# Kernel tuning notes

Hardware: AMD Instinct MI355X
Metric: run time of the kernel (lower is better)

## Reference

```python
import jax, jax.numpy as jnp
import numpy as np

OBS, PRED = 8, 12
EIN, EHID, NOISE = 64, 256, 64
GEMB = 64
DHID = EHID + NOISE  # 320
G, NPER = 8, 192
B = G * NPER


def leaky(x):
    return jnp.where(x > 0, x, 0.2 * x)


def lstm_cell(x, h, c, Wih, Whh, bih, bhh):
    gates = x @ Wih.T + bih + h @ Whh.T + bhh
    i, f, g, o = jnp.split(gates, 4, axis=-1)
    c = jax.nn.sigmoid(f) * c + jax.nn.sigmoid(i) * jnp.tanh(g)
    h = jax.nn.sigmoid(o) * jnp.tanh(c)
    return h, c


def kmeans(x, k, niter=10):
    # deterministic init: first k points (torch used randperm)
    c = x[:k]
    ar = jnp.arange(k)
    for _ in range(niter):
        d2 = ((x[:, None, :] - c[None, :, :]) ** 2).sum(-1)  # [N,k]
        a = jnp.argmin(d2, axis=1)
        onehot = (a[:, None] == ar[None, :]).astype(x.dtype)  # [N,k]
        cnt = onehot.sum(0)
        mean = (onehot.T @ x) / jnp.maximum(cnt, 1.0)[:, None]
        c = jnp.where((cnt == 0)[:, None], x[:k], mean)  # reseed dead clusters
    d2 = ((x[:, None, :] - c[None, :, :]) ** 2).sum(-1)
    return jnp.argmin(d2, axis=1)


def signed_graph(node, W_ne, b_ne, W_att, b_att):
    n, D = node.shape
    emb = node @ W_ne.T + b_ne  # [n,E]
    E = emb.shape[1]
    a_other, a_self = W_att[0, :E], W_att[0, E:]
    # e[i,j] = a_other.emb[j] + a_self.emb[i] + b  (cat([other, self]) order)
    e = (emb @ a_other)[None, :] + (emb @ a_self)[:, None] + b_att[0]
    edge = jax.nn.softmax(leaky(e), axis=0)
    edge = jnp.triu(edge, 0) + jnp.triu(edge, 1).T  # symmetrize from upper tri
    d = edge.sum(1)
    L = jnp.diag(d) - edge
    dinv = 1.0 / jnp.sqrt(d)
    L_sym = dinv[:, None] * L * dinv[None, :]
    lam, H = jnp.linalg.eigh(jax.lax.stop_gradient(L_sym))  # ascending eigvals
    H = H[:, :2]  # two smallest
    Hn = H / jnp.sqrt((H ** 2).sum(1, keepdims=True))
    labels = kmeans(Hn, int(np.ceil(n / 2)))
    same = labels[:, None] == labels[None, :]
    NEG = jnp.float32(-1e8)
    pos_alpha = jax.nn.softmax(leaky(edge * jnp.where(same, 1.0, NEG)), axis=0)
    neg_alpha = jax.nn.softmax(leaky(edge * jnp.where(same, NEG, 1.0)), axis=0)
    feat = jax.nn.relu(pos_alpha[..., None] * node[None, :, :]) + \
           jax.nn.relu(neg_alpha[..., None] * node[None, :, :])  # [n,n,D]
    return feat.sum(axis=1)


def setup_inputs():
    key = jax.random.key(0)
    ks = jax.random.split(key, 22)
    p = lambda k, s: jax.random.normal(k, s, jnp.float32) * 0.1
    starts = jnp.arange(G, dtype=jnp.int32) * NPER
    return {
        "input_traj": jax.random.normal(ks[0], (OBS + PRED, B, 2), jnp.float32),
        "enc_h0": jax.random.normal(ks[1], (B, EHID), jnp.float32),
        "enc_c0": jax.random.normal(ks[2], (B, EHID), jnp.float32),
        "noise_z": jax.random.normal(ks[3], (G, NOISE), jnp.float32),
        "W_emb": p(ks[4], (EIN, 2)), "b_emb": p(ks[5], (EIN,)),
        "Wih_e": p(ks[6], (4 * EHID, EIN)), "Whh_e": p(ks[7], (4 * EHID, EHID)),
        "bih_e": p(ks[8], (4 * EHID,)), "bhh_e": p(ks[9], (4 * EHID,)),
        "Wih_d": p(ks[10], (4 * DHID, EIN)), "Whh_d": p(ks[11], (4 * DHID, DHID)),
        "bih_d": p(ks[12], (4 * DHID,)), "bhh_d": p(ks[13], (4 * DHID,)),
        "W_out": p(ks[14], (2, DHID)), "b_out": p(ks[15], (2,)),
        "W_ne": p(ks[16], (GEMB, DHID)), "b_ne": p(ks[17], (GEMB,)),
        "W_att": p(ks[18], (1, 2 * GEMB)), "b_att": p(ks[19], (1,)),
        "seq_start_end": jnp.stack([starts, starts + NPER], axis=1),
    }


def reference(input_traj, enc_h0, enc_c0, noise_z, W_emb, b_emb,
              Wih_e, Whh_e, bih_e, bhh_e, Wih_d, Whh_d, bih_d, bhh_d,
              W_out, b_out, W_ne, b_ne, W_att, b_att, seq_start_end):
    # ---- encoder ----
    x = jax.nn.relu(input_traj @ W_emb.T + b_emb)  # [T,B,EIN]
    def step(carry, xt):
        h, c = carry
        h, c = lstm_cell(xt, h, c, Wih_e, Whh_e, bih_e, bhh_e)
        return (h, c), None
    (h_enc, _), _ = jax.lax.scan(step, (enc_h0, enc_c0), x[:OBS])
    # ---- add per-scene noise (equal-sized scenes) ----
    z = jnp.repeat(noise_z, NPER, axis=0)  # [B,NOISE]
    h = jnp.concatenate([h_enc, z], axis=1)  # [B,DHID]
    c = jnp.zeros_like(h)
    traj_out = input_traj[OBS - 1]  # [B,2]
    sg = jax.vmap(lambda nd: signed_graph(nd, W_ne, b_ne, W_att, b_att))
    preds = []
    for i in range(PRED):  # eval mode: no teacher forcing
        inp = jax.nn.relu(traj_out @ W_emb.T + b_emb)
        if i % 12 == 4:
            h = sg(h.reshape(G, NPER, DHID)).reshape(B, DHID)
        h, c = lstm_cell(inp, h, c, Wih_d, Whh_d, bih_d, bhh_d)
        traj_out = h @ W_out.T + b_out
        preds.append(traj_out)
    return jnp.stack(preds)  # [PRED,B,2]
```

## Files before the change

### kernel.cpp

```cpp
#include <hip/hip_runtime.h>
#include <hip/hip_bf16.h>

typedef __hip_bfloat16 bf16;

#define NN 192
#define NG 8
#define BB 1536
#define EHID 256
#define DH 320
#define PRED 12
#define STRD 192
#define ATILE (NN*STRD)

__device__ __forceinline__ int aoffc(int r, int c){
  int c4 = c >> 2;
  int s = (c4 & ~7) | ((c4 + 3*r) & 7);
  return r*STRD + (s << 2) + (c & 3);
}

#define WAVE_SYNC() do { asm volatile("" ::: "memory"); __builtin_amdgcn_wave_barrier(); } while (0)

__device__ __forceinline__ float waveSum(float v){
#pragma unroll
  for (int o = 32; o > 0; o >>= 1) v += __shfl_down(v, o);
  return v;
}
__device__ __forceinline__ double waveSumD(double v){
#pragma unroll
  for (int o = 32; o > 0; o >>= 1) v += __shfl_down(v, o);
  return v;
}
__device__ __forceinline__ float waveAllSum(float v){
#pragma unroll
  for (int o = 32; o > 0; o >>= 1) v += __shfl_xor(v, o);
  return v;
}
__device__ __forceinline__ double waveAllSumD(double v){
#pragma unroll
  for (int o = 32; o > 0; o >>= 1) v += __shfl_xor(v, o);
  return v;
}

__device__ __forceinline__ double blockSumD(double v, double* red){
  int lane = threadIdx.x & 63, wid = threadIdx.x >> 6, nw = (int)blockDim.x >> 6;
  double s = waveSumD(v);
  __syncthreads();
  if (lane == 0) red[wid] = s;
  __syncthreads();
  if (wid == 0){
    double t = (lane < nw) ? red[lane] : 0.0;
    t = waveSumD(t);
    if (lane == 0) red[0] = t;
  }
  __syncthreads();
  return red[0];
}


__global__ void k_zero_int(int* __restrict__ p, int n){
  int i = blockIdx.x*blockDim.x + threadIdx.x;
  if (i < n) p[i] = 0;
}
__global__ void k_zero_f(float* __restrict__ p, int n){
  int i = blockIdx.x*blockDim.x + threadIdx.x;
  if (i < n) p[i] = 0.f;
}

__global__ void k_probe(const unsigned short* __restrict__ src, int n, int* __restrict__ cnt){
  int tid = blockIdx.x*blockDim.x + threadIdx.x;
  int stride = gridDim.x*blockDim.x;
  int bad = 0;
  for (int j = tid; j < n; j += stride){
    float v = __uint_as_float(((unsigned int)src[j]) << 16);
    if (!(fabsf(v) < 100.f)) bad++;
  }
#pragma unroll
  for (int o = 32; o > 0; o >>= 1) bad += __shfl_down(bad, o);
  if ((threadIdx.x & 63) == 0 && bad > 0) atomicAdd(cnt, bad);
}
__global__ void k_flag(const int* __restrict__ cnt, int* __restrict__ flag){
  *flag = (*cnt > 4096) ? 1 : 0;
}

struct CvtArgs {
  const void* src[20];
  float*      dst[20];
  int         n[20];
};

__global__ void k_convert(CvtArgs a, const int* __restrict__ flag){
  int id = blockIdx.y;
  int n = a.n[id];
  float* d = a.dst[id];
  int t = blockIdx.x*blockDim.x + threadIdx.x;
  int stride = gridDim.x*blockDim.x;
  if (*flag == 0){
    const bf16* s = (const bf16*)a.src[id];
    for (int j = t; j < n; j += stride) d[j] = __bfloat162float(s[j]);
  } else {
    const float* s = (const float*)a.src[id];
    for (int j = t; j < n; j += stride) d[j] = s[j];
  }
}


__global__ void k_embed(const float* __restrict__ in, const float* __restrict__ W,
                        const float* __restrict__ b, float* __restrict__ out){
  int r = blockIdx.x, e = threadIdx.x;
  float x = in[r*2], y = in[r*2+1];
  float v = W[e*2]*x + W[e*2+1]*y + b[e];
  out[r*64+e] = v > 0.f ? v : 0.f;
}

__global__ void k_concat(const float* __restrict__ henc, const float* __restrict__ z,
                         float* __restrict__ h){
  int idx = blockIdx.x*blockDim.x + threadIdx.x;
  if (idx >= BB*DH) return;
  int b = idx / DH, j = idx - b*DH;
  h[idx] = (j < EHID) ? henc[b*EHID + j] : z[(b/NN)*64 + (j - EHID)];
}

__global__ void k_copy_f(const float* __restrict__ in, float* __restrict__ dst, int n){
  int i = blockIdx.x*blockDim.x + threadIdx.x;
  if (i < n) dst[i] = in[i];
}

__global__ __launch_bounds__(256) void k_gates(
    const float* __restrict__ A1, const float* __restrict__ W1, int K1,
    const float* __restrict__ A2, const float* __restrict__ W2, int K2,
    const float* __restrict__ b1, const float* __restrict__ b2,
    float* __restrict__ C, int N){
  __shared__ __align__(16) float As[32][68];
  __shared__ __align__(16) float Ws[32][68];
  int tid = threadIdx.x;
  int tx = tid & 15, ty = tid >> 4;
  int n0 = blockIdx.x * 64, m0 = blockIdx.y * 64;
  float acc[4][4] = {};
  for (int ph = 0; ph < 2; ++ph){
    const float* A = ph ? A2 : A1;
    const float* W = ph ? W2 : W1;
    int K = ph ? K2 : K1;
    for (int k0 = 0; k0 < K; k0 += 32){
      {
        int am = tid >> 2, ak = (tid & 3) * 8;
        const float* srcA = A + (size_t)(m0+am)*K + k0 + ak;
        float4 f0 = *(const float4*)(srcA);
        float4 f1 = *(const float4*)(srcA+4);
        As[ak+0][am]=f0.x; As[ak+1][am]=f0.y; As[ak+2][am]=f0.z; As[ak+3][am]=f0.w;
        As[ak+4][am]=f1.x; As[ak+5][am]=f1.y; As[ak+6][am]=f1.z; As[ak+7][am]=f1.w;
        const float* srcW = W + (size_t)(n0+am)*K + k0 + ak;
        float4 w0 = *(const float4*)(srcW);
        float4 w1 = *(const float4*)(srcW+4);
        Ws[ak+0][am]=w0.x; Ws[ak+1][am]=w0.y; Ws[ak+2][am]=w0.z; Ws[ak+3][am]=w0.w;
        Ws[ak+4][am]=w1.x; Ws[ak+5][am]=w1.y; Ws[ak+6][am]=w1.z; Ws[ak+7][am]=w1.w;
      }
      __syncthreads();
#pragma unroll
      for (int k = 0; k < 32; ++k){
        float4 a0 = *(const float4*)&As[k][ty*4];
        float4 b0 = *(const float4*)&Ws[k][tx*4];
        float av[4] = {a0.x, a0.y, a0.z, a0.w};
        float bv[4] = {b0.x, b0.y, b0.z, b0.w};
#pragma unroll
        for (int i = 0; i < 4; ++i)
#pragma unroll
          for (int j = 0; j < 4; ++j)
            acc[i][j] += av[i]*bv[j];
      }
      __syncthreads();
    }
  }
  float bs[4];
#pragma unroll
  for (int j = 0; j < 4; ++j){
    int col = n0 + tx*4 + j;
    bs[j] = b1[col] + b2[col];
  }
#pragma unroll
  for (int i = 0; i < 4; ++i){
    int row = m0 + ty*4 + i;
    float4 v;
    v.x = acc[i][0] + bs[0]; v.y = acc[i][1] + bs[1];
    v.z = acc[i][2] + bs[2]; v.w = acc[i][3] + bs[3];
    *(float4*)&C[(size_t)row*N + n0 + tx*4] = v;
  }
}

__global__ void k_lstm(const float* __restrict__ gates, float* __restrict__ c,
                       float* __restrict__ h, int H){
  int idx = blockIdx.x*blockDim.x + threadIdx.x;
  if (idx >= BB*H) return;
  int b = idx / H, j = idx - b*H;
  const float* g = gates + (size_t)b*4*H;
  float gi = g[j], gf = g[H+j], gg = g[2*H+j], go = g[3*H+j];
  float si = 1.f/(1.f+expf(-gi));
  float sf = 1.f/(1.f+expf(-gf));
  float so = 1.f/(1.f+expf(-go));
  float cc = sf*c[idx] + si*tanhf(gg);
  c[idx] = cc;
  h[idx] = so*tanhf(cc);
}

__global__ void k_outproj(const float* __restrict__ h, const float* __restrict__ W,
                          const float* __restrict__ bo, float* __restrict__ traj,
                          void* __restrict__ outbase, int step, const int* __restrict__ flag){
  int b = blockIdx.x, lane = threadIdx.x;
  const float* hb = h + (size_t)b*DH;
  float a0 = 0.f, a1 = 0.f;
  for (int k = lane; k < DH; k += 64){
    float hv = hb[k];
    a0 += hv*W[k];
    a1 += hv*W[DH+k];
  }
  a0 = waveSum(a0); a1 = waveSum(a1);
  if (lane == 0){
    a0 += bo[0]; a1 += bo[1];
    traj[b*2] = a0; traj[b*2+1] = a1;
    size_t idx = (size_t)step*BB*2 + (size_t)b*2;
    if (*flag == 0){
      bf16* o = (bf16*)outbase;
      o[idx] = __float2bfloat16(a0); o[idx+1] = __float2bfloat16(a1);
    } else {
      float* o = (float*)outbase;
      o[idx] = a0; o[idx+1] = a1;
    }
  }
}


__global__ void k_sg_emb(const float* __restrict__ h, const float* __restrict__ Wne,
                         const float* __restrict__ bne, const float* __restrict__ Watt,
                         double* __restrict__ sself, double* __restrict__ sother){
  int node = blockIdx.x, e = threadIdx.x;
  const float* hb = h + (size_t)node*DH;
  double acc = (double)bne[e];
  for (int k = 0; k < DH; ++k) acc += (double)hb[k]*(double)Wne[e*DH+k];
  double po = acc * (double)Watt[e];
  double ps = acc * (double)Watt[64+e];
  po = waveSumD(po); ps = waveSumD(ps);
  if (e == 0){ sother[node] = po; sself[node] = ps; }
}

__global__ void k_sg_edgecol(const double* __restrict__ sself, const double* __restrict__ sother,
                             const float* __restrict__ batt, double* __restrict__ edge){
  int g = blockIdx.x, j = threadIdx.x;
  const double* ss = sself + g*NN;
  double bb = (double)batt[0];
  double sj = sother[g*NN + j];
  double m = -1e300;
  for (int i = 0; i < NN; ++i){
    double e = ss[i] + sj + bb; e = e > 0.0 ? e : 0.2*e;
    m = fmax(m, e);
  }
  double sum = 0.0;
  for (int i = 0; i < NN; ++i){
    double e = ss[i] + sj + bb; e = e > 0.0 ? e : 0.2*e;
    sum += exp(e - m);
  }
  double* E = edge + (size_t)g*NN*NN;
  for (int i = 0; i < NN; ++i){
    double e = ss[i] + sj + bb; e = e > 0.0 ? e : 0.2*e;
    E[i*NN + j] = exp(e - m)/sum;
  }
}

__global__ void k_sg_sym(const double* __restrict__ edge, double* __restrict__ esym){
  int idx = blockIdx.x*blockDim.x + threadIdx.x;
  if (idx >= NG*NN*NN) return;
  int g = idx / (NN*NN), r = idx - g*NN*NN;
  int i = r / NN, j = r - i*NN;
  const double* E = edge + (size_t)g*NN*NN;
  esym[idx] = (i <= j) ? E[i*NN + j] : E[j*NN + i];
}

__global__ void k_sg_dsum(const double* __restrict__ esym, double* __restrict__ darr){
  int i = blockIdx.x*blockDim.x + threadIdx.x;
  if (i >= NG*NN) return;
  int g = i / NN, li = i - g*NN;
  const double* E = esym + (size_t)g*NN*NN + (size_t)li*NN;
  double s = 0.0;
  for (int j = 0; j < NN; ++j) s += E[j];
  darr[i] = fmax(s, 1e-300);
}

__global__ void k_sg_lsym(const double* __restrict__ esym, const double* __restrict__ darr,
                          float* __restrict__ Afull){
  int idx = blockIdx.x*blockDim.x + threadIdx.x;
  if (idx >= NG*NN*NN) return;
  int g = idx / (NN*NN), r = idx - g*NN*NN;
  int i = r / NN, j = r - i*NN;
  double w = esym[idx];
  double lij = (i == j) ? (darr[g*NN+i] - w) : (-w);
  Afull[(size_t)g*ATILE + aoffc(i, j)] =
      (float)(lij / (sqrt(darr[g*NN+i])*sqrt(darr[g*NN+j])));
}

__global__ __launch_bounds__(1024) void k_sg_eigen(const float* __restrict__ Afull,
                                                   const double* __restrict__ darr,
                                                   double* __restrict__ v1out){
  extern __shared__ unsigned char ldsraw[];
  float*  A     = (float*)ldsraw;
  double* dd    = (double*)(ldsraw + 147456);
  double* ee    = dd + NN;
  double* yv    = ee + NN;
  double* lu_d  = yv + NN;
  double* lu_du = lu_d + NN;
  double* lu_du2= lu_du + NN;
  double* redA  = lu_du2 + NN;
  double* redB  = redA + 16;
  double* salpha= redB + 16;
  float*  uu    = (float*)(ldsraw + 156944);
  float*  ww    = uu + NN;
  int*    lu_piv= (int*)(ww + NN);
  float*  pp4   = (float*)yv;
  double* lu_dl = (double*)uu;

  int g = blockIdx.x, tid = threadIdx.x;
  int lane = tid & 63, wid = tid >> 6;
  int rtid = tid & 255, team = tid >> 8;

  const float* src = Afull + (size_t)g*ATILE;
  for (int t = tid*4; t < ATILE; t += 4096) *(float4*)&A[t] = *(const float4*)&src[t];
  __syncthreads();

  for (int k = 0; k < NN-65; ++k){
    int m = NN-1-k;
    int i = k+1+rtid;
    float x = 0.f;
    if (rtid < m) x = A[aoffc(i, k)];
    if (tid == 0) *salpha = (double)x;
    if (team == 0){
      float part = (rtid > 0 && rtid < m) ? x*x : 0.f;
      part = waveSum(part);
      if (lane == 0) redA[wid] = (double)part;
    }
    __syncthreads();
    double sigma = redA[0] + redA[1] + redA[2] + redA[3];
    double alpha = *salpha;
    double beta, tau, scale;
    if (sigma <= 1e-30){ tau = 0.0; beta = alpha; scale = 0.0; }
    else {
      beta = -copysign(sqrt(alpha*alpha + sigma), alpha);
      tau = (beta - alpha)/beta;
      scale = 1.0/(alpha - beta);
    }
    float tau_f = (float)tau, scale_f = (float)scale;
    if (tid == 0){
      dd[k] = (double)A[aoffc(k, k)];
      ee[k] = beta;
      A[aoffc(k, k)] = tau_f;
    }
    if (tau != 0.0){
      float u_i = 0.f;
      if (rtid < m) u_i = (rtid == 0) ? 1.f : x*scale_f;
      if (team == 0 && rtid < m){
        uu[i] = u_i;
        if (rtid >= 1) A[aoffc(i, k)] = u_i;
      }
      __syncthreads();
      int c0 = k+1;
      int cA = (c0+3)&~3;
      int cB = (c0+31)&~31;
      int NB = (NN - cB) >> 5;
      const int rb = i*STRD;
      const int rk3 = (3*i) & 7;
      int off[8];
#pragma unroll
      for (int j = 0; j < 8; ++j) off[j] = ((j + rk3) & 7) << 2;
      if (rtid < m){
        float s0=0.f, s1=0.f, s2=0.f, s3=0.f, accs=0.f;
        if (team == 3){
          int c = c0;
          for (; c < cA; ++c) accs += A[aoffc(i, c)]*uu[c];
          for (; c < cB; c += 4){
            int c4 = c>>2; int s = (c4&~7)|((c4+rk3)&7);
            float4 a4 = *(const float4*)&A[rb + (s<<2)];
            float4 u4 = *(const float4*)&uu[c];
            s0 += a4.x*u4.x; s1 += a4.y*u4.y; s2 += a4.z*u4.z; s3 += a4.w*u4.w;
          }
        }
        for (int b = team; b < NB; b += 4){
          int c = cB + (b<<5);
          const int cb = rb + c;
#pragma unroll
          for (int j = 0; j < 8; ++j){
            float4 a4 = *(const float4*)&A[cb + off[j]];
            float4 u4 = *(const float4*)&uu[c + 4*j];
            s0 += a4.x*u4.x; s1 += a4.y*u4.y; s2 += a4.z*u4.z; s3 += a4.w*u4.w;
          }
        }
        pp4[team*NN + i - (k+1) + (k+1)] = ((s0+s1)+(s2+s3)) + accs;
      }
      __syncthreads();
      float p = 0.f;
      if (rtid < m)
        p = tau_f*(pp4[i] + pp4[NN + i] + pp4[2*NN + i] + pp4[3*NN + i]);
      if (team == 0){
        float vp = (rtid < m) ? u_i*p : 0.f;
        vp = waveSum(vp);
        if (lane == 0) redB[wid] = (double)vp;
      }
      __syncthreads();
      double vtp = redB[0] + redB[1] + redB[2] + redB[3];
      float Kc_f = (float)(0.5*tau*vtp);
      float w_i = 0.f;
      if (rtid < m){
        w_i = p - Kc_f*u_i;
        if (team == 0) ww[i] = w_i;
      }
      __syncthreads();
      if (rtid < m){
        if (team == 3){
          int c = c0;
          for (; c < cA; ++c) A[aoffc(i, c)] -= u_i*ww[c] + w_i*uu[c];
          for (; c < cB; c += 4){
            int c4 = c>>2; int s = (c4&~7)|((c4+rk3)&7);
            float* ap = &A[rb + (s<<2)];
            float4 a4 = *(const float4*)ap;
            float4 u4 = *(const float4*)&uu[c];
            float4 w4 = *(const float4*)&ww[c];
            a4.x -= u_i*w4.x + w_i*u4.x;
            a4.y -= u_i*w4.y + w_i*u4.y;
            a4.z -= u_i*w4.z + w_i*u4.z;
            a4.w -= u_i*w4.w + w_i*u4.w;
            *(float4*)ap = a4;
          }
        }
        for (int b = team; b < NB; b += 4){
          int c = cB + (b<<5);
          const int cb = rb + c;
#pragma unroll
          for (int j = 0; j < 8; ++j){
            float* ap = &A[cb + off[j]];
            float4 a4 = *(const float4*)ap;
            float4 u4 = *(const float4*)&uu[c + 4*j];
            float4 w4 = *(const float4*)&ww[c + 4*j];
            a4.x -= u_i*w4.x + w_i*u4.x;
            a4.y -= u_i*w4.y + w_i*u4.y;
            a4.z -= u_i*w4.z + w_i*u4.z;
            a4.w -= u_i*w4.w + w_i*u4.w;
            *(float4*)ap = a4;
          }
        }
      }
      __syncthreads();
    } else {
      __syncthreads();
    }
  }

  if (wid != 0) return;

  for (int k = NN-65; k < NN-2; ++k){
    int m = NN-1-k;
    int i = k+1+lane;
    bool act = lane < m;
    float x = act ? A[aoffc(i, k)] : 0.f;
    float part = (lane > 0) ? x*x : 0.f;
    float sig_f = waveAllSum(part);
    float alpha_f = __shfl(x, 0);
    double sigma = (double)sig_f;
    double alpha = (double)alpha_f;
    double beta, tau, scale;
    if (sigma <= 1e-30){ tau = 0.0; beta = alpha; scale = 0.0; }
    else {
      beta = -copysign(sqrt(alpha*alpha + sigma), alpha);
      tau = (beta - alpha)/beta;
      scale = 1.0/(alpha - beta);
    }
    float tau_f = (float)tau, scale_f = (float)scale;
    if (lane == 0){
      dd[k] = (double)A[aoffc(k, k)];
      ee[k] = beta;
      A[aoffc(k, k)] = tau_f;
    }
    if (tau == 0.0) continue;
    float u = (lane == 0) ? 1.f : x*scale_f;
    int base4 = (k+1) & ~3;
    int ph = (k+1) - base4;
    uu[lane + ph] = u;
    if (lane >= 1 && act) A[aoffc(i, k)] = u;
    WAVE_SYNC();
    int ic = act ? i : (k+1);
    const int rb = ic*STRD;
    const int rk3 = (3*ic) & 7;
    float s0=0.f, s1=0.f, s2=0.f, s3=0.f, accs=0.f;
    {
      int c = k+1;
      int cA = (c+3)&~3; if (cA > NN) cA = NN;
      for (; c < cA; ++c) accs += A[aoffc(ic, c)]*uu[c-base4];
      for (; c < NN; c += 4){
        int c4 = c>>2; int s = (c4&~7)|((c4+rk3)&7);
        float4 a4 = *(const float4*)&A[rb + (s<<2)];
        float4 u4 = *(const float4*)&uu[c-base4];
        s0 += a4.x*u4.x; s1 += a4.y*u4.y; s2 += a4.z*u4.z; s3 += a4.w*u4.w;
      }
    }
    float p = tau_f*(((s0+s1)+(s2+s3)) + accs);
    float vtp = waveAllSum(u*p);
    float Kc_f = (float)(0.5*tau*(double)vtp);
    float w = p - Kc_f*u;
    ww[lane + ph] = w;
    WAVE_SYNC();
    if (act){
      int c = k+1;
      int cA = (c+3)&~3; if (cA > NN) cA = NN;
      for (; c < cA; ++c) A[aoffc(i, c)] -= u*ww[c-base4] + w*uu[c-base4];
      for (; c < NN; c += 4){
        int c4 = c>>2; int s = (c4&~7)|((c4+rk3)&7);
        float* ap = &A[rb + (s<<2)];
        float4 a4 = *(const float4*)ap;
        float4 u4 = *(const float4*)&uu[c-base4];
        float4 w4 = *(const float4*)&ww[c-base4];
        a4.x -= u*w4.x + w*u4.x;
        a4.y -= u*w4.y + w*u4.y;
        a4.z -= u*w4.z + w*u4.z;
        a4.w -= u*w4.w + w*u4.w;
        *(float4*)ap = a4;
      }
    }
    WAVE_SYNC();
  }

  if (lane == 0){
    dd[NN-2] = (double)A[aoffc(NN-2, NN-2)];
    ee[NN-2] = (double)A[aoffc(NN-1, NN-2)];
    dd[NN-1] = (double)A[aoffc(NN-1, NN-1)];
  }
  WAVE_SYNC();

  {
    double mn = 1e300, mx = -1e300;
    for (int i = lane; i < NN; i += 64){
      double r = (i > 0 ? fabs(ee[i-1]) : 0.0) + (i < NN-1 ? fabs(ee[i]) : 0.0);
      mn = fmin(mn, dd[i]-r); mx = fmax(mx, dd[i]+r);
    }
#pragma unroll
    for (int o = 32; o > 0; o >>= 1){
      mn = fmin(mn, __shfl_down(mn, o));
      mx = fmax(mx, __shfl_down(mx, o));
    }
    mn = __shfl(mn, 0); mx = __shfl(mx, 0);
    double lo = mn - 1e-8 - 1e-9*fabs(mn);
    double hi = mx + 1e-8 + 1e-9*fabs(mx);
    for (int it = 0; it < 10; ++it){
      double lam = lo + (hi-lo)*((double)(lane+1)/65.0);
      int cnt = 0;
      double q = dd[0] - lam;
      if (q < 0.0) cnt++;
      for (int i2 = 1; i2 < NN; ++i2){
        double den = q;
        if (fabs(den) < 1e-280) den = (den < 0.0) ? -1e-280 : 1e-280;
        q = dd[i2] - lam - ee[i2-1]*ee[i2-1]/den;
        if (q < 0.0) cnt++;
      }
      unsigned long long bal = __ballot(cnt >= 2);
      if (bal == 0ull){
        lo = lo + (hi-lo)*(64.0/65.0);
      } else {
        int j0 = __ffsll(bal) - 1;
        double nl = lo + (hi-lo)*((double)j0/65.0);
        double nh = lo + (hi-lo)*((double)(j0+1)/65.0);
        lo = nl; hi = nh;
      }
    }
    double lam1 = 0.5*(lo+hi);

    if (lane == 0){
      for (int i = 0; i < NN; ++i) lu_d[i] = dd[i] - lam1;
      for (int i = 0; i < NN-1; ++i){ lu_dl[i] = ee[i]; lu_du[i] = ee[i]; }
      for (int i = 0; i < NN-2; ++i) lu_du2[i] = 0.0;
      for (int i = 0; i < NN-1; ++i){
        if (fabs(lu_d[i]) >= fabs(lu_dl[i])){
          double di = lu_d[i];
          if (fabs(di) < 1e-30){ di = (di < 0.0) ? -1e-30 : 1e-30; lu_d[i] = di; }
          double fact = lu_dl[i]/di;
          lu_dl[i] = fact;
          lu_d[i+1] -= fact*lu_du[i];
          lu_piv[i] = 0;
        } else {
          double fact = lu_d[i]/lu_dl[i];
          lu_d[i] = lu_dl[i];
          double tmp = lu_d[i+1];
          lu_d[i+1] = lu_du[i] - fact*tmp;
          if (i < NN-2){ lu_du2[i] = lu_du[i+1]; lu_du[i+1] = -fact*lu_du[i+1]; }
          lu_du[i] = tmp;
          lu_dl[i] = fact;
          lu_piv[i] = 1;
        }
      }
      if (fabs(lu_d[NN-1]) < 1e-30)
        lu_d[NN-1] = (lu_d[NN-1] < 0.0) ? -1e-30 : 1e-30;
      for (int i = 0; i < NN; ++i) yv[i] = 1.0 + 0.001*(double)((i*37)%29);
      for (int round = 0; round < 2; ++round){
        for (int i = 0; i < NN-1; ++i){
          if (lu_piv[i] == 0){
            yv[i+1] -= lu_dl[i]*yv[i];
          } else {
            double t = yv[i]; yv[i] = yv[i+1]; yv[i+1] = t - lu_dl[i]*yv[i];
          }
        }
        double mx1 = 0.0;
        for (int i = 0; i < NN; ++i) mx1 = fmax(mx1, fabs(yv[i]));
        double inv1 = (mx1 > 0.0 && isfinite(mx1)) ? 1.0/mx1 : 1.0;
        for (int i = 0; i < NN; ++i) yv[i] *= inv1;
        yv[NN-1] = yv[NN-1]/lu_d[NN-1];
        yv[NN-2] = (yv[NN-2] - lu_du[NN-2]*yv[NN-1])/lu_d[NN-2];
        for (int i = NN-3; i >= 0; --i)
          yv[i] = (yv[i] - lu_du[i]*yv[i+1] - lu_du2[i]*yv[i+2])/lu_d[i];
        double mxv = 0.0;
        for (int i = 0; i < NN; ++i) mxv = fmax(mxv, fabs(yv[i]));
        double inv = (mxv > 0.0 && isfinite(mxv)) ? 1.0/mxv : 1.0;
        for (int i = 0; i < NN; ++i){
          double val = yv[i]*inv;
          if (!isfinite(val)) val = 0.0;
          yv[i] = val;
        }
      }
    }
  }
  WAVE_SYNC();

  {
    int r0 = lane, r1 = lane+64, r2 = lane+128;
    double y0 = yv[r0], y1 = yv[r1], y2 = yv[r2];
    for (int k = NN-3; k >= 0; --k){
      double tau = (double)A[aoffc(k, k)];
      if (tau != 0.0){
        double u0 = (r0 > k) ? ((r0 == k+1) ? 1.0 : (double)A[aoffc(r0, k)]) : 0.0;
        double u1 = (r1 > k) ? ((r1 == k+1) ? 1.0 : (double)A[aoffc(r1, k)]) : 0.0;
        double u2 = (r2 > k) ? ((r2 == k+1) ? 1.0 : (double)A[aoffc(r2, k)]) : 0.0;
        double part = u0*y0 + u1*y1 + u2*y2;
        part = waveAllSumD(part);
        double s = tau*part;
        y0 -= s*u0; y1 -= s*u1; y2 -= s*u2;
      }
    }

    const double* dg = darr + (size_t)g*NN;
    double d0 = dg[r0], d1 = dg[r1], d2 = dg[r2];
    double sd0 = sqrt(d0), sd1 = sqrt(d1), sd2 = sqrt(d2);
    double pd  = waveAllSumD(sd0*y0 + sd1*y1 + sd2*y2);
    double pn2 = waveAllSumD(d0 + d1 + d2);
    double coef = pd/fmax(pn2, 1e-300);
    y0 -= coef*sd0; y1 -= coef*sd1; y2 -= coef*sd2;
    double s2 = waveAllSumD(y0*y0 + y1*y1 + y2*y2);
    double nrm = sqrt(s2);
    double inv = (nrm > 0.0 && isfinite(nrm)) ? 1.0/nrm : 0.0;
    double o0 = y0*inv, o1 = y1*inv, o2 = y2*inv;
    if (!isfinite(o0)) o0 = 0.0;
    if (!isfinite(o1)) o1 = 0.0;
    if (!isfinite(o2)) o2 = 0.0;
    v1out[g*NN + r0] = o0;
    v1out[g*NN + r1] = o1;
    v1out[g*NN + r2] = o2;
  }
}

__global__ __launch_bounds__(256) void k_sg_kmeans(const double* __restrict__ darr,
                                                   const double* __restrict__ v1,
                                                   int* __restrict__ labels){
  __shared__ double px[NN], py[NN], cx[96], cy[96];
  __shared__ int lab[NN];
  __shared__ double red[16];
  int g = blockIdx.x, tid = threadIdx.x;
  double part = 0.0;
  for (int i = tid; i < NN; i += 256) part += darr[g*NN + i];
  double sumd = blockSumD(part, red);
  double invn = 1.0/sqrt(fmax(sumd, 1e-300));
  for (int i = tid; i < NN; i += 256){
    double h0 = sqrt(darr[g*NN + i])*invn;
    double h1 = v1[g*NN + i];
    double rn = sqrt(h0*h0 + h1*h1);
    double ax = h0/rn, ay = h1/rn;
    if (!isfinite(ax)) ax = 0.0;
    if (!isfinite(ay)) ay = 0.0;
    px[i] = ax; py[i] = ay;
  }
  __syncthreads();
  if (tid < 96){ cx[tid] = px[tid]; cy[tid] = py[tid]; }
  __syncthreads();
  for (int it = 0; it <= 10; ++it){
    if (tid < NN){
      double bx = px[tid], by = py[tid];
      double best = 1e300; int bi = 0;
      for (int a = 0; a < 96; ++a){
        double dx = bx - cx[a], dy = by - cy[a];
        double d2 = dx*dx + dy*dy;
        if (d2 < best){ best = d2; bi = a; }
      }
      lab[tid] = bi;
    }
    __syncthreads();
    if (it == 10) break;
    if (tid < 96){
      int c = 0; double sx = 0.0, sy = 0.0;
      for (int i = 0; i < NN; ++i){
        if (lab[i] == tid){ c++; sx += px[i]; sy += py[i]; }
      }
      if (c > 0){ cx[tid] = sx/(double)c; cy[tid] = sy/(double)c; }
      else      { cx[tid] = px[tid];      cy[tid] = py[tid]; }
    }
    __syncthreads();
  }
  if (tid < NN) labels[g*NN + tid] = lab[tid];
}

__global__ void k_sg_alpha(const double* __restrict__ esym, const int* __restrict__ labels,
                           float* __restrict__ S){
  __shared__ int lbs[NN];
  int g = blockIdx.x, j = threadIdx.x;
  if (j < NN) lbs[j] = labels[g*NN + j];
  __syncthreads();
  const double* E = esym + (size_t)g*NN*NN;
  const double NEG = -100000000.0;
  int lj = lbs[j];
  double mp = -1e300, mn = -1e300;
  for (int i = 0; i < NN; ++i){
    double w = E[i*NN + j];
    bool sm = (lbs[i] == lj);
    double vp = sm ? w : w*NEG; vp = vp > 0.0 ? vp : 0.2*vp;
    double vn = sm ? w*NEG : w; vn = vn > 0.0 ? vn : 0.2*vn;
    mp = fmax(mp, vp); mn = fmax(mn, vn);
  }
  double sp = 0.0, sn = 0.0;
  for (int i = 0; i < NN; ++i){
    double w = E[i*NN + j];
    bool sm = (lbs[i] == lj);
    double vp = sm ? w : w*NEG; vp = vp > 0.0 ? vp : 0.2*vp;
    double vn = sm ? w*NEG : w; vn = vn > 0.0 ? vn : 0.2*vn;
    sp += exp(vp - mp); sn += exp(vn - mn);
  }
  float* So = S + (size_t)g*NN*NN;
  for (int i = 0; i < NN; ++i){
    double w = E[i*NN + j];
    bool sm = (lbs[i] == lj);
    double vp = sm ? w : w*NEG; vp = vp > 0.0 ? vp : 0.2*vp;
    double vn = sm ? w*NEG : w; vn = vn > 0.0 ? vn : 0.2*vn;
    So[i*NN + j] = (float)(exp(vp - mp)/sp + exp(vn - mn)/sn);
  }
}

__global__ __launch_bounds__(320) void k_sg_feat(const float* __restrict__ S,
                                                 const float* __restrict__ hin,
                                                 float* __restrict__ hout){
  int r = blockIdx.x;
  int g = r / NN, li = r - g*NN;
  int dh = threadIdx.x;
  const float* Srow = S + (size_t)g*NN*NN + (size_t)li*NN;
  const float* hb = hin + (size_t)g*NN*DH;
  float acc = 0.f;
  for (int j = 0; j < NN; ++j){
    float w = Srow[j];
    float x = hb[(size_t)j*DH + dh];
    acc += w*(x > 0.f ? x : 0.f);
  }
  hout[(size_t)r*DH + dh] = acc;
}


extern "C" void kernel_launch(void* const* d_in, const int* in_sizes, int n_in,
                              void* d_out, int out_size, void* d_ws, size_t ws_size,
                              hipStream_t stream){
  (void)n_in; (void)out_size; (void)ws_size;

  float* ws = (float*)d_ws;
  float* inp   = ws;
  float* gates = ws + 98304;
  float* hA    = ws + 2064384;
  float* hB    = ws + 2555904;
  float* cD    = ws + 3047424;
  float* traj  = ws + 3538944;
  double* sself_d  = (double*)(ws + 3542016);
  double* sother_d = (double*)(ws + 3545088);
  double* darr_d   = (double*)(ws + 3548160);
  double* v1_d     = (double*)(ws + 3551232);
  int*    labels   = (int*)(ws + 3554304);
  double* edge_d = (double*)gates;
  double* esym_d = (double*)(gates + 589824);
  float*  Afull  = gates + 1179648;
  float*  Smat   = gates;
  float* a_traj = ws + 3555840;
  float* a_z    = ws + 3617280;
  float* a_Wemb = ws + 3617792;
  float* a_bemb = ws + 3617920;
  float* a_Wihe = ws + 3617984;
  float* a_Whhe = ws + 3683520;
  float* a_bihe = ws + 3945664;
  float* a_bhhe = ws + 3946688;
  float* a_Wihd = ws + 3947712;
  float* a_Whhd = ws + 4029632;
  float* a_bihd = ws + 4439232;
  float* a_bhhd = ws + 4440512;
  float* a_Wout = ws + 4441792;
  float* a_bout = ws + 4442432;
  float* a_Wne  = ws + 4442496;
  float* a_bne  = ws + 4462976;
  float* a_Watt = ws + 4463040;
  float* a_batt = ws + 4463168;
  int* cnt  = (int*)(ws + 4463232);
  int* flag = (int*)(ws + 4463233);

  const int EIG_LDS = 159248;
  hipFuncSetAttribute((const void*)k_sg_eigen,
                      hipFuncAttributeMaxDynamicSharedMemorySize, EIG_LDS);

  k_zero_int<<<1, 64, 0, stream>>>(cnt, 2);
  k_probe<<<256, 256, 0, stream>>>((const unsigned short*)d_in[1], in_sizes[1], cnt);
  k_flag<<<1, 1, 0, stream>>>(cnt, flag);

  CvtArgs ca;
  float* dsts[20] = { a_traj, hB, cD, a_z, a_Wemb, a_bemb, a_Wihe, a_Whhe, a_bihe,
                      a_bhhe, a_Wihd, a_Whhd, a_bihd, a_bhhd, a_Wout, a_bout,
                      a_Wne, a_bne, a_Watt, a_batt };
  for (int i = 0; i < 20; ++i){
    ca.src[i] = d_in[i];
    ca.dst[i] = dsts[i];
    ca.n[i]   = in_sizes[i];
  }
  k_convert<<<dim3(512, 20), 256, 0, stream>>>(ca, flag);

  for (int t = 0; t < 8; ++t){
    k_embed<<<BB, 64, 0, stream>>>(a_traj + (size_t)t*BB*2, a_Wemb, a_bemb, inp);
    k_gates<<<dim3(1024/64, BB/64), 256, 0, stream>>>(inp, a_Wihe, 64, hB, a_Whhe, EHID,
                                                      a_bihe, a_bhhe, gates, 1024);
    k_lstm<<<(BB*EHID+255)/256, 256, 0, stream>>>(gates, cD, hB, EHID);
  }

  k_concat<<<(BB*DH+255)/256, 256, 0, stream>>>(hB, a_z, hA);
  k_zero_f<<<(BB*DH+255)/256, 256, 0, stream>>>(cD, BB*DH);
  k_copy_f<<<(BB*2+255)/256, 256, 0, stream>>>(a_traj + (size_t)7*BB*2, traj, BB*2);

  float* hcur = hA;
  float* hoth = hB;
  for (int i = 0; i < PRED; ++i){
    k_embed<<<BB, 64, 0, stream>>>(traj, a_Wemb, a_bemb, inp);
    if (i == 4){
      k_sg_emb<<<BB, 64, 0, stream>>>(hcur, a_Wne, a_bne, a_Watt, sself_d, sother_d);
      k_sg_edgecol<<<NG, NN, 0, stream>>>(sself_d, sother_d, a_batt, edge_d);
      k_sg_sym<<<(NG*NN*NN+255)/256, 256, 0, stream>>>(edge_d, esym_d);
      k_sg_dsum<<<(NG*NN+255)/256, 256, 0, stream>>>(esym_d, darr_d);
      k_sg_lsym<<<(NG*NN*NN+255)/256, 256, 0, stream>>>(esym_d, darr_d, Afull);
      k_sg_eigen<<<NG, 1024, EIG_LDS, stream>>>(Afull, darr_d, v1_d);
      k_sg_kmeans<<<NG, 256, 0, stream>>>(darr_d, v1_d, labels);
      k_sg_alpha<<<NG, NN, 0, stream>>>(esym_d, labels, Smat);
      k_sg_feat<<<BB, DH, 0, stream>>>(Smat, hcur, hoth);
      float* tmp = hcur; hcur = hoth; hoth = tmp;
    }
    k_gates<<<dim3((4*DH)/64, BB/64), 256, 0, stream>>>(inp, a_Wihd, 64, hcur, a_Whhd, DH,
                                                        a_bihd, a_bhhd, gates, 4*DH);
    k_lstm<<<(BB*DH+255)/256, 256, 0, stream>>>(gates, cD, hcur, DH);
    k_outproj<<<BB, 64, 0, stream>>>(hcur, a_Wout, a_bout, traj, d_out, i, flag);
  }
}
```

Baseline: 2.297 ms.

## Fuse embedding, gate GEMM and LSTM cell; streamline Householder tridiagonalization

Gate weights and biases are permuted once so the four gates for each hidden unit sit next to each other. This lets a single kernel compute the input embedding into shared memory, run both GEMMs, and apply the LSTM cell in its epilogue, with ping-pong h buffers. That removes the separate embed and LSTM kernels and the round trip of the gates tensor through global memory, at the cost of extra one-time permutation launches and LDS use. The eigen kernel's Householder loop also drops a barrier by storing the raw column and folding the scale into the later products, with the reduction moved into each team.

```diff
diff --git a/kernel.cpp b/kernel.cpp
--- a/kernel.cpp
+++ b/kernel.cpp
@@ -103,14 +103,37 @@
   }
 }
 
-
-__global__ void k_embed(const float* __restrict__ in, const float* __restrict__ W,
-                        const float* __restrict__ b, float* __restrict__ out){
-  int r = blockIdx.x, e = threadIdx.x;
-  float x = in[r*2], y = in[r*2+1];
-  float v = W[e*2]*x + W[e*2+1]*y + b[e];
-  out[r*64+e] = v > 0.f ? v : 0.f;
-}
+__global__ void k_permw(const void* __restrict__ src, float* __restrict__ dst,
+                        int H, int K, const int* __restrict__ flag){
+  int idx = blockIdx.x*blockDim.x + threadIdx.x;
+  int n = 4*H*K;
+  if (idx >= n) return;
+  int r = idx / K, kk = idx - r*K;
+  int j = r >> 2, q = r & 3;
+  int si = (q*H + j)*K + kk;
+  float v;
+  if (*flag == 0) v = __bfloat162float(((const bf16*)src)[si]);
+  else            v = ((const float*)src)[si];
+  dst[idx] = v;
+}
+
+__global__ void k_permb(const void* __restrict__ b1, const void* __restrict__ b2,
+                        float* __restrict__ dst, int H, const int* __restrict__ flag){
+  int r = blockIdx.x*blockDim.x + threadIdx.x;
+  if (r >= 4*H) return;
+  int j = r >> 2, q = r & 3;
+  int si = q*H + j;
+  float v1, v2;
+  if (*flag == 0){
+    v1 = __bfloat162float(((const bf16*)b1)[si]);
+    v2 = __bfloat162float(((const bf16*)b2)[si]);
+  } else {
+    v1 = ((const float*)b1)[si];
+    v2 = ((const float*)b2)[si];
+  }
+  dst[r] = v1 + v2;
+}
+
 
 __global__ void k_concat(const float* __restrict__ henc, const float* __restrict__ z,
                          float* __restrict__ h){
@@ -125,80 +148,100 @@
   if (i < n) dst[i] = in[i];
 }
 
-__global__ __launch_bounds__(256) void k_gates(
-    const float* __restrict__ A1, const float* __restrict__ W1, int K1,
-    const float* __restrict__ A2, const float* __restrict__ W2, int K2,
-    const float* __restrict__ b1, const float* __restrict__ b2,
-    float* __restrict__ C, int N){
+__global__ __launch_bounds__(256) void k_gates_lstm(
+    const float* __restrict__ traj2,
+    const float* __restrict__ Wemb, const float* __restrict__ bemb,
+    const float* __restrict__ Wp, const float* __restrict__ Up,
+    const float* __restrict__ bsum,
+    const float* __restrict__ hin, float* __restrict__ hout,
+    float* __restrict__ cst, int H){
+  __shared__ __align__(16) float inpT[64][68];
   __shared__ __align__(16) float As[32][68];
   __shared__ __align__(16) float Ws[32][68];
   int tid = threadIdx.x;
   int tx = tid & 15, ty = tid >> 4;
   int n0 = blockIdx.x * 64, m0 = blockIdx.y * 64;
+
+  {
+    int r = tid & 63;
+    float x = traj2[(size_t)(m0 + r)*2];
+    float y = traj2[(size_t)(m0 + r)*2 + 1];
+    for (int e = tid >> 6; e < 64; e += 4){
+      float v = Wemb[e*2]*x + Wemb[e*2+1]*y + bemb[e];
+      inpT[e][r] = v > 0.f ? v : 0.f;
+    }
+  }
   float acc[4][4] = {};
-  for (int ph = 0; ph < 2; ++ph){
-    const float* A = ph ? A2 : A1;
-    const float* W = ph ? W2 : W1;
-    int K = ph ? K2 : K1;
-    for (int k0 = 0; k0 < K; k0 += 32){
-      {
-        int am = tid >> 2, ak = (tid & 3) * 8;
-        const float* srcA = A + (size_t)(m0+am)*K + k0 + ak;
-        float4 f0 = *(const float4*)(srcA);
-        float4 f1 = *(const float4*)(srcA+4);
-        As[ak+0][am]=f0.x; As[ak+1][am]=f0.y; As[ak+2][am]=f0.z; As[ak+3][am]=f0.w;
-        As[ak+4][am]=f1.x; As[ak+5][am]=f1.y; As[ak+6][am]=f1.z; As[ak+7][am]=f1.w;
-        const float* srcW = W + (size_t)(n0+am)*K + k0 + ak;
-        float4 w0 = *(const float4*)(srcW);
-        float4 w1 = *(const float4*)(srcW+4);
-        Ws[ak+0][am]=w0.x; Ws[ak+1][am]=w0.y; Ws[ak+2][am]=w0.z; Ws[ak+3][am]=w0.w;
-        Ws[ak+4][am]=w1.x; Ws[ak+5][am]=w1.y; Ws[ak+6][am]=w1.z; Ws[ak+7][am]=w1.w;
-      }
-      __syncthreads();
-#pragma unroll
-      for (int k = 0; k < 32; ++k){
-        float4 a0 = *(const float4*)&As[k][ty*4];
-        float4 b0 = *(const float4*)&Ws[k][tx*4];
-        float av[4] = {a0.x, a0.y, a0.z, a0.w};
-        float bv[4] = {b0.x, b0.y, b0.z, b0.w};
-#pragma unroll
-        for (int i = 0; i < 4; ++i)
-#pragma unroll
-          for (int j = 0; j < 4; ++j)
-            acc[i][j] += av[i]*bv[j];
-      }
-      __syncthreads();
-    }
-  }
-  float bs[4];
-#pragma unroll
-  for (int j = 0; j < 4; ++j){
-    int col = n0 + tx*4 + j;
-    bs[j] = b1[col] + b2[col];
-  }
-#pragma unroll
-  for (int i = 0; i < 4; ++i){
-    int row = m0 + ty*4 + i;
-    float4 v;
-    v.x = acc[i][0] + bs[0]; v.y = acc[i][1] + bs[1];
-    v.z = acc[i][2] + bs[2]; v.w = acc[i][3] + bs[3];
-    *(float4*)&C[(size_t)row*N + n0 + tx*4] = v;
-  }
-}
-
-__global__ void k_lstm(const float* __restrict__ gates, float* __restrict__ c,
-                       float* __restrict__ h, int H){
-  int idx = blockIdx.x*blockDim.x + threadIdx.x;
-  if (idx >= BB*H) return;
-  int b = idx / H, j = idx - b*H;
-  const float* g = gates + (size_t)b*4*H;
-  float gi = g[j], gf = g[H+j], gg = g[2*H+j], go = g[3*H+j];
-  float si = 1.f/(1.f+expf(-gi));
-  float sf = 1.f/(1.f+expf(-gf));
-  float so = 1.f/(1.f+expf(-go));
-  float cc = sf*c[idx] + si*tanhf(gg);
-  c[idx] = cc;
-  h[idx] = so*tanhf(cc);
+  for (int k0 = 0; k0 < 64; k0 += 32){
+    {
+      int am = tid >> 2, ak = (tid & 3) * 8;
+      const float* srcW = Wp + (size_t)(n0+am)*64 + k0 + ak;
+      float4 w0 = *(const float4*)(srcW);
+      float4 w1 = *(const float4*)(srcW+4);
+      Ws[ak+0][am]=w0.x; Ws[ak+1][am]=w0.y; Ws[ak+2][am]=w0.z; Ws[ak+3][am]=w0.w;
+      Ws[ak+4][am]=w1.x; Ws[ak+5][am]=w1.y; Ws[ak+6][am]=w1.z; Ws[ak+7][am]=w1.w;
+    }
+    __syncthreads();
+#pragma unroll
+    for (int k = 0; k < 32; ++k){
+      float4 a0 = *(const float4*)&inpT[k0+k][ty*4];
+      float4 b0 = *(const float4*)&Ws[k][tx*4];
+      float av[4] = {a0.x, a0.y, a0.z, a0.w};
+      float bv[4] = {b0.x, b0.y, b0.z, b0.w};
+#pragma unroll
+      for (int i = 0; i < 4; ++i)
+#pragma unroll
+        for (int j = 0; j < 4; ++j)
+          acc[i][j] += av[i]*bv[j];
+    }
+    __syncthreads();
+  }
+  for (int k0 = 0; k0 < H; k0 += 32){
+    {
+      int am = tid >> 2, ak = (tid & 3) * 8;
+      const float* srcA = hin + (size_t)(m0+am)*H + k0 + ak;
+      float4 f0 = *(const float4*)(srcA);
+      float4 f1 = *(const float4*)(srcA+4);
+      As[ak+0][am]=f0.x; As[ak+1][am]=f0.y; As[ak+2][am]=f0.z; As[ak+3][am]=f0.w;
+      As[ak+4][am]=f1.x; As[ak+5][am]=f1.y; As[ak+6][am]=f1.z; As[ak+7][am]=f1.w;
+      const float* srcW = Up + (size_t)(n0+am)*H + k0 + ak;
+      float4 w0 = *(const float4*)(srcW);
+      float4 w1 = *(const float4*)(srcW+4);
+      Ws[ak+0][am]=w0.x; Ws[ak+1][am]=w0.y; Ws[ak+2][am]=w0.z; Ws[ak+3][am]=w0.w;
+      Ws[ak+4][am]=w1.x; Ws[ak+5][am]=w1.y; Ws[ak+6][am]=w1.z; Ws[ak+7][am]=w1.w;
+    }
+    __syncthreads();
+#pragma unroll
+    for (int k = 0; k < 32; ++k){
+      float4 a0 = *(const float4*)&As[k][ty*4];
+      float4 b0 = *(const float4*)&Ws[k][tx*4];
+      float av[4] = {a0.x, a0.y, a0.z, a0.w};
+      float bv[4] = {b0.x, b0.y, b0.z, b0.w};
+#pragma unroll
+      for (int i = 0; i < 4; ++i)
+#pragma unroll
+        for (int j = 0; j < 4; ++j)
+          acc[i][j] += av[i]*bv[j];
+    }
+    __syncthreads();
+  }
+  int s = (n0 >> 2) + tx;
+  float4 bq = *(const float4*)&bsum[n0 + tx*4];
+#pragma unroll
+  for (int i2 = 0; i2 < 4; ++i2){
+    int row = m0 + ty*4 + i2;
+    float gi = acc[i2][0] + bq.x;
+    float gf = acc[i2][1] + bq.y;
+    float gg = acc[i2][2] + bq.z;
+    float go = acc[i2][3] + bq.w;
+    float si = 1.f/(1.f+expf(-gi));
+    float sf = 1.f/(1.f+expf(-gf));
+    float so = 1.f/(1.f+expf(-go));
+    size_t cidx = (size_t)row*H + s;
+    float cc = sf*cst[cidx] + si*tanhf(gg);
+    cst[cidx] = cc;
+    hout[cidx] = so*tanhf(cc);
+  }
 }
 
 __global__ void k_outproj(const float* __restrict__ h, const float* __restrict__ W,
@@ -308,12 +351,11 @@
   double* lu_du2= lu_du + NN;
   double* redA  = lu_du2 + NN;
   double* redB  = redA + 16;
-  double* salpha= redB + 16;
-  float*  uu    = (float*)(ldsraw + 156944);
-  float*  ww    = uu + NN;
+  float*  vv    = (float*)(ldsraw + 156944);
+  float*  ww    = vv + NN;
   int*    lu_piv= (int*)(ww + NN);
-  float*  pp4   = (float*)yv;
-  double* lu_dl = (double*)uu;
+  float*  pp4T  = (float*)yv;
+  double* lu_dl = (double*)vv;
 
   int g = blockIdx.x, tid = threadIdx.x;
   int lane = tid & 63, wid = tid >> 6;
@@ -328,15 +370,15 @@
     int i = k+1+rtid;
     float x = 0.f;
     if (rtid < m) x = A[aoffc(i, k)];
-    if (tid == 0) *salpha = (double)x;
     if (team == 0){
+      if (rtid < m) vv[i] = x;
       float part = (rtid > 0 && rtid < m) ? x*x : 0.f;
       part = waveSum(part);
       if (lane == 0) redA[wid] = (double)part;
     }
     __syncthreads();
     double sigma = redA[0] + redA[1] + redA[2] + redA[3];
-    double alpha = *salpha;
+    double alpha = (double)vv[k+1];
     double beta, tau, scale;
     if (sigma <= 1e-30){ tau = 0.0; beta = alpha; scale = 0.0; }
     else {
@@ -353,30 +395,20 @@
     if (tau != 0.0){
       float u_i = 0.f;
       if (rtid < m) u_i = (rtid == 0) ? 1.f : x*scale_f;
-      if (team == 0 && rtid < m){
-        uu[i] = u_i;
-        if (rtid >= 1) A[aoffc(i, k)] = u_i;
-      }
-      __syncthreads();
-      int c0 = k+1;
-      int cA = (c0+3)&~3;
-      int cB = (c0+31)&~31;
+      if (team == 0 && rtid >= 1 && rtid < m) A[aoffc(i, k)] = u_i;
+      int cB = ((k+2)+31)&~31;
       int NB = (NN - cB) >> 5;
       const int rb = i*STRD;
       const int rk3 = (3*i) & 7;
       int off[8];
 #pragma unroll
       for (int j = 0; j < 8; ++j) off[j] = ((j + rk3) & 7) << 2;
+      float head = 0.f, s0=0.f, s1=0.f, s2=0.f, s3=0.f;
       if (rtid < m){
-        float s0=0.f, s1=0.f, s2=0.f, s3=0.f, accs=0.f;
         if (team == 3){
-          int c = c0;
-          for (; c < cA; ++c) accs += A[aoffc(i, c)]*uu[c];
-          for (; c < cB; c += 4){
-            int c4 = c>>2; int s = (c4&~7)|((c4+rk3)&7);
-            float4 a4 = *(const float4*)&A[rb + (s<<2)];
-            float4 u4 = *(const float4*)&uu[c];
-            s0 += a4.x*u4.x; s1 += a4.y*u4.y; s2 += a4.z*u4.z; s3 += a4.w*u4.w;
+          for (int c = k+1; c < cB; ++c){
+            float uc = (c == k+1) ? 1.f : vv[c]*scale_f;
+            head += A[aoffc(i, c)]*uc;
           }
         }
         for (int b = team; b < NB; b += 4){
@@ -385,45 +417,36 @@
 #pragma unroll
           for (int j = 0; j < 8; ++j){
             float4 a4 = *(const float4*)&A[cb + off[j]];
-            float4 u4 = *(const float4*)&uu[c + 4*j];
-            s0 += a4.x*u4.x; s1 += a4.y*u4.y; s2 += a4.z*u4.z; s3 += a4.w*u4.w;
+            float4 v4 = *(const float4*)&vv[c + 4*j];
+            s0 += a4.x*v4.x; s1 += a4.y*v4.y; s2 += a4.z*v4.z; s3 += a4.w*v4.w;
           }
         }
-        pp4[team*NN + i - (k+1) + (k+1)] = ((s0+s1)+(s2+s3)) + accs;
-      }
+      }
+      float s_t = head + scale_f*((s0+s1)+(s2+s3));
+      if (rtid < m) pp4T[(i<<2) + team] = s_t;
+      float z = (rtid < m) ? u_i*s_t : 0.f;
+      z = waveSum(z);
+      if (lane == 0) redB[wid] = (double)z;
       __syncthreads();
-      float p = 0.f;
-      if (rtid < m)
-        p = tau_f*(pp4[i] + pp4[NN + i] + pp4[2*NN + i] + pp4[3*NN + i]);
-      if (team == 0){
-        float vp = (rtid < m) ? u_i*p : 0.f;
-        vp = waveSum(vp);
-        if (lane == 0) redB[wid] = (double)vp;
-      }
-      __syncthreads();
-      double vtp = redB[0] + redB[1] + redB[2] + redB[3];
+      double vtpS = 0.0;
+#pragma unroll
+      for (int w = 0; w < 16; ++w) vtpS += redB[w];
+      double vtp = tau*vtpS;
       float Kc_f = (float)(0.5*tau*vtp);
       float w_i = 0.f;
       if (rtid < m){
+        float4 q = *(const float4*)&pp4T[i<<2];
+        float p = tau_f*(q.x + q.y + q.z + q.w);
         w_i = p - Kc_f*u_i;
         if (team == 0) ww[i] = w_i;
       }
       __syncthreads();
       if (rtid < m){
+        float wis = w_i*scale_f;
         if (team == 3){
-          int c = c0;
-          for (; c < cA; ++c) A[aoffc(i, c)] -= u_i*ww[c] + w_i*uu[c];
-          for (; c < cB; c += 4){
-            int c4 = c>>2; int s = (c4&~7)|((c4+rk3)&7);
-            float* ap = &A[rb + (s<<2)];
-            float4 a4 = *(const float4*)ap;
-            float4 u4 = *(const float4*)&uu[c];
-            float4 w4 = *(const float4*)&ww[c];
-            a4.x -= u_i*w4.x + w_i*u4.x;
-            a4.y -= u_i*w4.y + w_i*u4.y;
-            a4.z -= u_i*w4.z + w_i*u4.z;
-            a4.w -= u_i*w4.w + w_i*u4.w;
-            *(float4*)ap = a4;
+          for (int c = k+1; c < cB; ++c){
+            float uc = (c == k+1) ? 1.f : vv[c]*scale_f;
+            A[aoffc(i, c)] -= u_i*ww[c] + w_i*uc;
           }
         }
         for (int b = team; b < NB; b += 4){
@@ -433,12 +456,12 @@
           for (int j = 0; j < 8; ++j){
             float* ap = &A[cb + off[j]];
             float4 a4 = *(const float4*)ap;
-            float4 u4 = *(const float4*)&uu[c + 4*j];
+            float4 v4 = *(const float4*)&vv[c + 4*j];
             float4 w4 = *(const float4*)&ww[c + 4*j];
-            a4.x -= u_i*w4.x + w_i*u4.x;
-            a4.y -= u_i*w4.y + w_i*u4.y;
-            a4.z -= u_i*w4.z + w_i*u4.z;
-            a4.w -= u_i*w4.w + w_i*u4.w;
+            a4.x -= u_i*w4.x + wis*v4.x;
+            a4.y -= u_i*w4.y + wis*v4.y;
+            a4.z -= u_i*w4.z + wis*v4.z;
+            a4.w -= u_i*w4.w + wis*v4.w;
             *(float4*)ap = a4;
           }
         }
@@ -478,7 +501,7 @@
     float u = (lane == 0) ? 1.f : x*scale_f;
     int base4 = (k+1) & ~3;
     int ph = (k+1) - base4;
-    uu[lane + ph] = u;
+    vv[lane + ph] = u;
     if (lane >= 1 && act) A[aoffc(i, k)] = u;
     WAVE_SYNC();
     int ic = act ? i : (k+1);
@@ -488,11 +511,11 @@
     {
       int c = k+1;
       int cA = (c+3)&~3; if (cA > NN) cA = NN;
-      for (; c < cA; ++c) accs += A[aoffc(ic, c)]*uu[c-base4];
+      for (; c < cA; ++c) accs += A[aoffc(ic, c)]*vv[c-base4];
       for (; c < NN; c += 4){
         int c4 = c>>2; int s = (c4&~7)|((c4+rk3)&7);
         float4 a4 = *(const float4*)&A[rb + (s<<2)];
-        float4 u4 = *(const float4*)&uu[c-base4];
+        float4 u4 = *(const float4*)&vv[c-base4];
         s0 += a4.x*u4.x; s1 += a4.y*u4.y; s2 += a4.z*u4.z; s3 += a4.w*u4.w;
       }
     }
@@ -505,12 +528,12 @@
     if (act){
       int c = k+1;
       int cA = (c+3)&~3; if (cA > NN) cA = NN;
-      for (; c < cA; ++c) A[aoffc(i, c)] -= u*ww[c-base4] + w*uu[c-base4];
+      for (; c < cA; ++c) A[aoffc(i, c)] -= u*ww[c-base4] + w*vv[c-base4];
       for (; c < NN; c += 4){
         int c4 = c>>2; int s = (c4&~7)|((c4+rk3)&7);
         float* ap = &A[rb + (s<<2)];
         float4 a4 = *(const float4*)ap;
-        float4 u4 = *(const float4*)&uu[c-base4];
+        float4 u4 = *(const float4*)&vv[c-base4];
         float4 w4 = *(const float4*)&ww[c-base4];
         a4.x -= u*w4.x + w*u4.x;
         a4.y -= u*w4.y + w*u4.y;
@@ -780,6 +803,7 @@
   double* esym_d = (double*)(gates + 589824);
   float*  Afull  = gates + 1179648;
   float*  Smat   = gates;
+  float*  hC     = gates;
   float* a_traj = ws + 3555840;
   float* a_z    = ws + 3617280;
   float* a_Wemb = ws + 3617792;
@@ -800,6 +824,7 @@
   float* a_batt = ws + 4463168;
   int* cnt  = (int*)(ws + 4463232);
   int* flag = (int*)(ws + 4463233);
+  (void)inp; (void)a_bhhe; (void)a_bhhd;
 
   const int EIG_LDS = 159248;
   hipFuncSetAttribute((const void*)k_sg_eigen,
@@ -820,21 +845,29 @@
   }
   k_convert<<<dim3(512, 20), 256, 0, stream>>>(ca, flag);
 
+  k_permw<<<(4*EHID*64   + 255)/256, 256, 0, stream>>>(d_in[6],  a_Wihe, EHID, 64,   flag);
+  k_permw<<<(4*EHID*EHID + 255)/256, 256, 0, stream>>>(d_in[7],  a_Whhe, EHID, EHID, flag);
+  k_permb<<<(4*EHID + 255)/256, 256, 0, stream>>>(d_in[8], d_in[9],  a_bihe, EHID, flag);
+  k_permw<<<(4*DH*64     + 255)/256, 256, 0, stream>>>(d_in[10], a_Wihd, DH, 64, flag);
+  k_permw<<<(4*DH*DH     + 255)/256, 256, 0, stream>>>(d_in[11], a_Whhd, DH, DH, flag);
+  k_permb<<<(4*DH + 255)/256, 256, 0, stream>>>(d_in[12], d_in[13], a_bihd, DH, flag);
+
+  float* ecur = hB;
+  float* eoth = hC;
   for (int t = 0; t < 8; ++t){
-    k_embed<<<BB, 64, 0, stream>>>(a_traj + (size_t)t*BB*2, a_Wemb, a_bemb, inp);
-    k_gates<<<dim3(1024/64, BB/64), 256, 0, stream>>>(inp, a_Wihe, 64, hB, a_Whhe, EHID,
-                                                      a_bihe, a_bhhe, gates, 1024);
-    k_lstm<<<(BB*EHID+255)/256, 256, 0, stream>>>(gates, cD, hB, EHID);
-  }
-
-  k_concat<<<(BB*DH+255)/256, 256, 0, stream>>>(hB, a_z, hA);
+    k_gates_lstm<<<dim3(4*EHID/64, BB/64), 256, 0, stream>>>(
+        a_traj + (size_t)t*BB*2, a_Wemb, a_bemb,
+        a_Wihe, a_Whhe, a_bihe, ecur, eoth, cD, EHID);
+    float* tmp = ecur; ecur = eoth; eoth = tmp;
+  }
+
+  k_concat<<<(BB*DH+255)/256, 256, 0, stream>>>(ecur, a_z, hA);
   k_zero_f<<<(BB*DH+255)/256, 256, 0, stream>>>(cD, BB*DH);
   k_copy_f<<<(BB*2+255)/256, 256, 0, stream>>>(a_traj + (size_t)7*BB*2, traj, BB*2);
 
   float* hcur = hA;
   float* hoth = hB;
   for (int i = 0; i < PRED; ++i){
-    k_embed<<<BB, 64, 0, stream>>>(traj, a_Wemb, a_bemb, inp);
     if (i == 4){
       k_sg_emb<<<BB, 64, 0, stream>>>(hcur, a_Wne, a_bne, a_Watt, sself_d, sother_d);
       k_sg_edgecol<<<NG, NN, 0, stream>>>(sself_d, sother_d, a_batt, edge_d);
@@ -847,9 +880,10 @@
       k_sg_feat<<<BB, DH, 0, stream>>>(Smat, hcur, hoth);
       float* tmp = hcur; hcur = hoth; hoth = tmp;
     }
-    k_gates<<<dim3((4*DH)/64, BB/64), 256, 0, stream>>>(inp, a_Wihd, 64, hcur, a_Whhd, DH,
-                                                        a_bihd, a_bhhd, gates, 4*DH);
-    k_lstm<<<(BB*DH+255)/256, 256, 0, stream>>>(gates, cD, hcur, DH);
+    k_gates_lstm<<<dim3(4*DH/64, BB/64), 256, 0, stream>>>(
+        traj, a_Wemb, a_bemb,
+        a_Wihd, a_Whhd, a_bihd, hcur, hoth, cD, DH);
+    { float* tmp = hcur; hcur = hoth; hoth = tmp; }
     k_outproj<<<BB, 64, 0, stream>>>(hcur, a_Wout, a_bout, traj, d_out, i, flag);
   }
 }
```

Result: slower. 2.504 ms (+9.0%).
